# Kernel tuning notes

Measured on AMD Instinct MI355X. Metric: run time of the kernel, lower is better.

## Reference

```python
import jax, jax.numpy as jnp
import numpy as np
from jax import lax

OC = 128
KH, KW = 2, 2


def setup_inputs() -> dict:
    key = jax.random.key(0)
    k1, k2, k3 = jax.random.split(key, 3)
    C = 256
    n = C * KH * KW
    stdv = 1.0 / np.sqrt(n)
    x = jax.random.normal(k1, (16, C, 64, 64), dtype=jnp.float32)
    # original allocates (oc^2*kh*kw, C, kh, kw) but only uses first oc*kh*kw rows
    weight = jax.random.uniform(k2, (OC * OC * KH * KW, C, KH, KW), dtype=jnp.float32,
                                minval=-stdv, maxval=stdv)
    bias = jax.random.uniform(k3, (OC * (KH + KW),), dtype=jnp.float32,
                              minval=-stdv, maxval=stdv)
    return {"x": x, "weight": weight, "bias": bias}


def _robin_shuffle(x, weight, bias):
    # output[b,z,p,q] = stride-1 valid conv at (p,q) using filter
    # index (p%KH)*KW + (q%KW) + z*KH*KW, plus matching bias.
    nf = OC * KH * KW
    w = weight[:nf]  # (nf, C, KH, KW)
    full = lax.conv_general_dilated(
        x, w, window_strides=(1, 1), padding='VALID',
        dimension_numbers=('NCHW', 'OIHW', 'NCHW'))  # (N, nf, H', W')
    full = full + bias[:nf][None, :, None, None]
    N, _, Hp, Wp = full.shape
    full = full.reshape(N, OC, KH * KW, Hp, Wp)
    idx = (jnp.arange(Hp)[:, None] % KH) * KW + (jnp.arange(Wp)[None, :] % KW)  # (H', W')
    out = jnp.take_along_axis(full, idx[None, None, None, :, :], axis=2)
    return out.squeeze(2)  # (N, OC, H', W')


def reference(x, weight, bias):
    return _robin_shuffle(x, weight, bias)
```

## Files before the change

kernel.cpp:

```cpp
#include <hip/hip_runtime.h>

typedef __bf16 v8bf __attribute__((ext_vector_type(8)));
typedef float f32x4 __attribute__((ext_vector_type(4)));

#define C_IN 256
#define HW   64
#define OHW  63
#define NOC  128

__global__ void wprep(const float* __restrict__ w, __bf16* __restrict__ Wf) {
  int f = blockIdx.x;
  int c = threadIdx.x;
  f32x4 v = *(const f32x4*)(w + (size_t)f * 1024 + c * 4);
  int oc = f >> 2, kp = f & 3;
#pragma unroll
  for (int khkw = 0; khkw < 4; ++khkw)
    Wf[(((size_t)(kp * 4 + khkw) * 32 + (c >> 3)) * 128 + oc) * 8 + (c & 7)] =
        (__bf16)v[khkw];
}

__global__ __launch_bounds__(1024, 4) void robin_main(
    const float* __restrict__ x, const __bf16* __restrict__ Wf,
    const float* __restrict__ bias, float* __restrict__ out) {
  __shared__ __align__(16) __bf16 xs[2][5 * 33 * 64];
  char* xb0 = (char*)xs[0];
  char* xb1 = (char*)xs[1];

  const int tid  = threadIdx.x;
  const int lane = tid & 63;
  const int wid  = tid >> 6;
  const int hb   = blockIdx.x;
  const int n    = blockIdx.y;
  const int h0   = hb * 4;

  const int ocg  = wid >> 2;
  const int kp   = wid & 3;
  const int ph   = kp >> 1, pw = kp & 1;
  const int lcol = lane & 15;
  const int lg   = lane >> 4;

  if (tid < 80) {
    int g  = tid & 7;
    int t2 = tid >> 3;
    int dy = t2 % 5, bi = t2 / 5;
    f32x4 z = {0.f, 0.f, 0.f, 0.f};
    *(f32x4*)((bi ? xb1 : xb0) + (dy * 33 + 32) * 128 + g * 16) = z;
  }

  int boff[4];
#pragma unroll
  for (int khkw = 0; khkw < 4; ++khkw) {
    int kh = khkw >> 1, kw = khkw & 1;
    int dy0  = ph + kh;
    int wcol = 2 * lcol + pw + kw;
    int wp_  = wcol >> 1;
    boff[khkw] = ((dy0 * 33 + wp_) * 128 + (wcol & 1) * 64 + lg * 16) ^
                 ((wp_ & 7) << 4);
  }

  f32x4 acc[2][4];
#pragma unroll
  for (int m = 0; m < 2; ++m)
#pragma unroll
    for (int f = 0; f < 4; ++f) acc[m][f] = (f32x4){0.f, 0.f, 0.f, 0.f};

  const float* xbase = x + (size_t)n * C_IN * HW * HW;
  f32x4 xr[3];
  v8bf  a_reg[4][2];

#define A_LOAD(QQ)                                                             \
  {                                                                            \
    _Pragma("unroll") for (int khkw = 0; khkw < 4; ++khkw) {                   \
      const __bf16* wp =                                                       \
          Wf + (((size_t)(kp * 4 + khkw) * 32 + (QQ) * 4 + lg) * 128 +        \
                ocg * 32 + lcol) * 8;                                          \
      a_reg[khkw][0] = *(const v8bf*)wp;                                       \
      a_reg[khkw][1] = *(const v8bf*)(wp + 128);                               \
    }                                                                          \
  }

#define LOADQ(QQ)                                                              \
  {                                                                            \
    const int cbase = (QQ) * 32;                                               \
    _Pragma("unroll") for (int k = 0; k < 3; ++k) {                            \
      int v = k * 1024 + tid;                                                  \
      if (v < 2560) {                                                          \
        int w4 = v & 15, c = (v >> 4) & 31, dy = v >> 9;                       \
        int y = h0 + dy;                                                       \
        if (y < HW)                                                            \
          xr[k] = *(const f32x4*)(xbase + ((size_t)(cbase + c) * HW + y) * HW +\
                                  w4 * 4);                                     \
        else                                                                   \
          xr[k] = (f32x4){0.f, 0.f, 0.f, 0.f};                                 \
      }                                                                        \
    }                                                                          \
  }

#define WRITEQ(QQ)                                                             \
  {                                                                            \
    char* xd = ((QQ) & 1) ? xb1 : xb0;                                         \
    _Pragma("unroll") for (int k = 0; k < 3; ++k) {                            \
      int v = k * 1024 + tid;                                                  \
      if (v < 2560) {                                                          \
        int w4 = v & 15, c = (v >> 4) & 31, dy = v >> 9;                       \
        _Pragma("unroll") for (int j = 0; j < 4; ++j) {                        \
          int wcol = w4 * 4 + j;                                               \
          int wp_  = wcol >> 1;                                                \
          int bo = ((dy * 33 + wp_) * 128 + (wcol & 1) * 64 + c * 2) ^         \
                   ((wp_ & 7) << 4);                                           \
          *(__bf16*)(xd + bo) = (__bf16)xr[k][j];                              \
        }                                                                      \
      }                                                                        \
    }                                                                          \
  }

  LOADQ(0);
  WRITEQ(0);
  __syncthreads();

  for (int q = 0; q < 8; ++q) {
    A_LOAD(q);
    if (q < 7) LOADQ(q + 1);

    {
      const char* xsb = (q & 1) ? xb1 : xb0;
#pragma unroll
      for (int khkw = 0; khkw < 4; ++khkw) {
        v8bf b[4];
#pragma unroll
        for (int r = 0; r < 2; ++r)
#pragma unroll
          for (int hh = 0; hh < 2; ++hh)
            b[r * 2 + hh] =
                *(const v8bf*)(xsb + boff[khkw] + r * 8448 + hh * 2048);

#pragma unroll
        for (int m = 0; m < 2; ++m)
#pragma unroll
          for (int f = 0; f < 4; ++f)
            acc[m][f] = __builtin_amdgcn_mfma_f32_16x16x32_bf16(
                a_reg[khkw][m], b[f], acc[m][f], 0, 0, 0);
      }
    }

    if (q < 7) {
      WRITEQ(q + 1);
      __syncthreads();
    }
  }

#pragma unroll
  for (int m = 0; m < 2; ++m) {
#pragma unroll
    for (int r = 0; r < 2; ++r) {
      const int h = h0 + 2 * r + ph;
#pragma unroll
      for (int hh = 0; hh < 2; ++hh) {
        const int w = 2 * (hh * 16 + lcol) + pw;
        f32x4 v = acc[m][r * 2 + hh];
        if (h < OHW && w < OHW) {
#pragma unroll
          for (int reg = 0; reg < 4; ++reg) {
            int oc = ocg * 32 + m * 16 + lg * 4 + reg;
            out[((size_t)(n * NOC + oc) * OHW + h) * OHW + w] =
                v[reg] + bias[oc * 4 + kp];
          }
        }
      }
    }
  }
#undef A_LOAD
#undef LOADQ
#undef WRITEQ
}

extern "C" void kernel_launch(void* const* d_in, const int* in_sizes, int n_in,
                              void* d_out, int out_size, void* d_ws, size_t ws_size,
                              hipStream_t stream) {
  const float* x      = (const float*)d_in[0];
  const float* weight = (const float*)d_in[1];
  const float* bias   = (const float*)d_in[2];
  float* out          = (float*)d_out;
  __bf16* Wf          = (__bf16*)d_ws;

  wprep<<<512, 256, 0, stream>>>(weight, Wf);
  robin_main<<<dim3(16, 16), 1024, 0, stream>>>(x, Wf, bias, out);
}
```

Before: 44.65 us.

## Halve row strip per block, widen per-wave OC tile, raise MFMA priority

Each block now covers a 2-row strip (3 input rows staged in LDS) with 512 threads. Each wave computes 64 output channels instead of 32, so it holds 4 A fragments and needs only 2 B fragments per tap. The grid doubles to 32x16 blocks, which is meant to improve occupancy and load balance across CUs. The cost is more halo re-reading of input rows and more weight reloads per output. s_setprio is raised around the MFMA bursts.

```diff
diff --git a/kernel.cpp b/kernel.cpp
--- a/kernel.cpp
+++ b/kernel.cpp
@@ -19,19 +19,19 @@
         (__bf16)v[khkw];
 }
 
-__global__ __launch_bounds__(1024, 4) void robin_main(
+__global__ __launch_bounds__(512, 4) void robin_main(
     const float* __restrict__ x, const __bf16* __restrict__ Wf,
     const float* __restrict__ bias, float* __restrict__ out) {
-  __shared__ __align__(16) __bf16 xs[2][5 * 33 * 64];
+  __shared__ __align__(16) __bf16 xs[2][3 * 33 * 64];
   char* xb0 = (char*)xs[0];
   char* xb1 = (char*)xs[1];
 
-  const int tid  = threadIdx.x;
-  const int lane = tid & 63;
-  const int wid  = tid >> 6;
-  const int hb   = blockIdx.x;
-  const int n    = blockIdx.y;
-  const int h0   = hb * 4;
+  const int tid   = threadIdx.x;
+  const int lane  = tid & 63;
+  const int wid   = tid >> 6;
+  const int strip = blockIdx.x;
+  const int n     = blockIdx.y;
+  const int h0    = strip * 2;
 
   const int ocg  = wid >> 2;
   const int kp   = wid & 3;
@@ -39,43 +39,44 @@
   const int lcol = lane & 15;
   const int lg   = lane >> 4;
 
-  if (tid < 80) {
-    int g  = tid & 7;
-    int t2 = tid >> 3;
-    int dy = t2 % 5, bi = t2 / 5;
+  if (tid < 48) {
+    int bi = tid / 24, r2 = tid % 24;
+    int k = r2 >> 3, g = r2 & 7;
     f32x4 z = {0.f, 0.f, 0.f, 0.f};
-    *(f32x4*)((bi ? xb1 : xb0) + (dy * 33 + 32) * 128 + g * 16) = z;
+    *(f32x4*)((bi ? xb1 : xb0) + (k * 33 + 32) * 128 + g * 16) = z;
   }
 
   int boff[4];
 #pragma unroll
   for (int khkw = 0; khkw < 4; ++khkw) {
     int kh = khkw >> 1, kw = khkw & 1;
-    int dy0  = ph + kh;
+    int dy   = ph + kh;
     int wcol = 2 * lcol + pw + kw;
     int wp_  = wcol >> 1;
-    boff[khkw] = ((dy0 * 33 + wp_) * 128 + (wcol & 1) * 64 + lg * 16) ^
+    boff[khkw] = ((dy * 33 + wp_) * 128 + (wcol & 1) * 64 + lg * 16) ^
                  ((wp_ & 7) << 4);
   }
 
-  f32x4 acc[2][4];
+  f32x4 acc[4][2];
 #pragma unroll
-  for (int m = 0; m < 2; ++m)
+  for (int m = 0; m < 4; ++m)
 #pragma unroll
-    for (int f = 0; f < 4; ++f) acc[m][f] = (f32x4){0.f, 0.f, 0.f, 0.f};
+    for (int f = 0; f < 2; ++f) acc[m][f] = (f32x4){0.f, 0.f, 0.f, 0.f};
 
   const float* xbase = x + (size_t)n * C_IN * HW * HW;
+  const int s_c  = tid >> 4;
+  const int s_w4 = tid & 15;
   f32x4 xr[3];
-  v8bf  a_reg[4][2];
+  v8bf  a_reg[4][4];
 
 #define A_LOAD(QQ)                                                             \
   {                                                                            \
     _Pragma("unroll") for (int khkw = 0; khkw < 4; ++khkw) {                   \
       const __bf16* wp =                                                       \
           Wf + (((size_t)(kp * 4 + khkw) * 32 + (QQ) * 4 + lg) * 128 +        \
-                ocg * 32 + lcol) * 8;                                          \
-      a_reg[khkw][0] = *(const v8bf*)wp;                                       \
-      a_reg[khkw][1] = *(const v8bf*)(wp + 128);                               \
+                ocg * 64 + lcol) * 8;                                          \
+      _Pragma("unroll") for (int m = 0; m < 4; ++m)                            \
+          a_reg[khkw][m] = *(const v8bf*)(wp + m * 128);                       \
     }                                                                          \
   }
 
@@ -83,16 +84,12 @@
   {                                                                            \
     const int cbase = (QQ) * 32;                                               \
     _Pragma("unroll") for (int k = 0; k < 3; ++k) {                            \
-      int v = k * 1024 + tid;                                                  \
-      if (v < 2560) {                                                          \
-        int w4 = v & 15, c = (v >> 4) & 31, dy = v >> 9;                       \
-        int y = h0 + dy;                                                       \
-        if (y < HW)                                                            \
-          xr[k] = *(const f32x4*)(xbase + ((size_t)(cbase + c) * HW + y) * HW +\
-                                  w4 * 4);                                     \
-        else                                                                   \
-          xr[k] = (f32x4){0.f, 0.f, 0.f, 0.f};                                 \
-      }                                                                        \
+      int y = h0 + k;                                                          \
+      if (y < HW)                                                              \
+        xr[k] = *(const f32x4*)(xbase + ((size_t)(cbase + s_c) * HW + y) * HW +\
+                                s_w4 * 4);                                     \
+      else                                                                     \
+        xr[k] = (f32x4){0.f, 0.f, 0.f, 0.f};                                   \
     }                                                                          \
   }
 
@@ -100,16 +97,12 @@
   {                                                                            \
     char* xd = ((QQ) & 1) ? xb1 : xb0;                                         \
     _Pragma("unroll") for (int k = 0; k < 3; ++k) {                            \
-      int v = k * 1024 + tid;                                                  \
-      if (v < 2560) {                                                          \
-        int w4 = v & 15, c = (v >> 4) & 31, dy = v >> 9;                       \
-        _Pragma("unroll") for (int j = 0; j < 4; ++j) {                        \
-          int wcol = w4 * 4 + j;                                               \
-          int wp_  = wcol >> 1;                                                \
-          int bo = ((dy * 33 + wp_) * 128 + (wcol & 1) * 64 + c * 2) ^         \
-                   ((wp_ & 7) << 4);                                           \
-          *(__bf16*)(xd + bo) = (__bf16)xr[k][j];                              \
-        }                                                                      \
+      _Pragma("unroll") for (int j = 0; j < 4; ++j) {                          \
+        int wcol = s_w4 * 4 + j;                                               \
+        int wp_  = wcol >> 1;                                                  \
+        int bo = ((k * 33 + wp_) * 128 + (wcol & 1) * 64 + s_c * 2) ^          \
+                 ((wp_ & 7) << 4);                                             \
+        *(__bf16*)(xd + bo) = (__bf16)xr[k][j];                                \
       }                                                                        \
     }                                                                          \
   }
@@ -126,20 +119,19 @@
       const char* xsb = (q & 1) ? xb1 : xb0;
 #pragma unroll
       for (int khkw = 0; khkw < 4; ++khkw) {
-        v8bf b[4];
+        v8bf b[2];
 #pragma unroll
-        for (int r = 0; r < 2; ++r)
+        for (int hh = 0; hh < 2; ++hh)
+          b[hh] = *(const v8bf*)(xsb + boff[khkw] + hh * 2048);
+
+        __builtin_amdgcn_s_setprio(1);
 #pragma unroll
-          for (int hh = 0; hh < 2; ++hh)
-            b[r * 2 + hh] =
-                *(const v8bf*)(xsb + boff[khkw] + r * 8448 + hh * 2048);
-
+        for (int m = 0; m < 4; ++m)
 #pragma unroll
-        for (int m = 0; m < 2; ++m)
-#pragma unroll
-          for (int f = 0; f < 4; ++f)
+          for (int f = 0; f < 2; ++f)
             acc[m][f] = __builtin_amdgcn_mfma_f32_16x16x32_bf16(
                 a_reg[khkw][m], b[f], acc[m][f], 0, 0, 0);
+        __builtin_amdgcn_s_setprio(0);
       }
     }
 
@@ -149,19 +141,18 @@
     }
   }
 
+  const int h = h0 + ph;
+  if (h < OHW) {
 #pragma unroll
-  for (int m = 0; m < 2; ++m) {
-#pragma unroll
-    for (int r = 0; r < 2; ++r) {
-      const int h = h0 + 2 * r + ph;
+    for (int m = 0; m < 4; ++m) {
 #pragma unroll
       for (int hh = 0; hh < 2; ++hh) {
         const int w = 2 * (hh * 16 + lcol) + pw;
-        f32x4 v = acc[m][r * 2 + hh];
-        if (h < OHW && w < OHW) {
+        f32x4 v = acc[m][hh];
+        if (w < OHW) {
 #pragma unroll
           for (int reg = 0; reg < 4; ++reg) {
-            int oc = ocg * 32 + m * 16 + lg * 4 + reg;
+            int oc = ocg * 64 + m * 16 + lg * 4 + reg;
             out[((size_t)(n * NOC + oc) * OHW + h) * OHW + w] =
                 v[reg] + bias[oc * 4 + kp];
           }
@@ -184,5 +175,5 @@
   __bf16* Wf          = (__bf16*)d_ws;
 
   wprep<<<512, 256, 0, stream>>>(weight, Wf);
-  robin_main<<<dim3(16, 16), 1024, 0, stream>>>(x, Wf, bias, out);
+  robin_main<<<dim3(32, 16), 512, 0, stream>>>(x, Wf, bias, out);
 }
```

New measurement: 79.65 us. +78.4%, slower.

## Deepen global-to-register prefetch to two stages with fully unrolled channel loop

Applied to the files above, without the earlier changes.

Adds a second register staging buffer so global loads for chunk q+2 are issued while chunk q is computed and chunk q+1 is written to LDS. The channel loop is fully unrolled so the compiler can pick buffers statically. This hides more global-load latency at the cost of 12 extra VGPRs per thread, which may lower occupancy under the 1024x4 launch bounds or cause spills.

```diff
diff --git a/kernel.cpp b/kernel.cpp
--- a/kernel.cpp
+++ b/kernel.cpp
@@ -65,7 +65,7 @@
     for (int f = 0; f < 4; ++f) acc[m][f] = (f32x4){0.f, 0.f, 0.f, 0.f};
 
   const float* xbase = x + (size_t)n * C_IN * HW * HW;
-  f32x4 xr[3];
+  f32x4 xrA[3], xrB[3];
   v8bf  a_reg[4][2];
 
 #define A_LOAD(QQ)                                                             \
@@ -79,7 +79,7 @@
     }                                                                          \
   }
 
-#define LOADQ(QQ)                                                              \
+#define LOADQ(QQ, XR)                                                          \
   {                                                                            \
     const int cbase = (QQ) * 32;                                               \
     _Pragma("unroll") for (int k = 0; k < 3; ++k) {                            \
@@ -88,15 +88,15 @@
         int w4 = v & 15, c = (v >> 4) & 31, dy = v >> 9;                       \
         int y = h0 + dy;                                                       \
         if (y < HW)                                                            \
-          xr[k] = *(const f32x4*)(xbase + ((size_t)(cbase + c) * HW + y) * HW +\
+          XR[k] = *(const f32x4*)(xbase + ((size_t)(cbase + c) * HW + y) * HW +\
                                   w4 * 4);                                     \
         else                                                                   \
-          xr[k] = (f32x4){0.f, 0.f, 0.f, 0.f};                                 \
+          XR[k] = (f32x4){0.f, 0.f, 0.f, 0.f};                                 \
       }                                                                        \
     }                                                                          \
   }
 
-#define WRITEQ(QQ)                                                             \
+#define WRITEQ(QQ, XR)                                                         \
   {                                                                            \
     char* xd = ((QQ) & 1) ? xb1 : xb0;                                         \
     _Pragma("unroll") for (int k = 0; k < 3; ++k) {                            \
@@ -108,46 +108,52 @@
           int wp_  = wcol >> 1;                                                \
           int bo = ((dy * 33 + wp_) * 128 + (wcol & 1) * 64 + c * 2) ^         \
                    ((wp_ & 7) << 4);                                           \
-          *(__bf16*)(xd + bo) = (__bf16)xr[k][j];                              \
+          *(__bf16*)(xd + bo) = (__bf16)XR[k][j];                              \
         }                                                                      \
       }                                                                        \
     }                                                                          \
   }
 
-  LOADQ(0);
-  WRITEQ(0);
+#define COMPUTE(QQ)                                                            \
+  {                                                                            \
+    const char* xsb = ((QQ) & 1) ? xb1 : xb0;                                  \
+    _Pragma("unroll") for (int khkw = 0; khkw < 4; ++khkw) {                   \
+      v8bf b[4];                                                               \
+      _Pragma("unroll") for (int r = 0; r < 2; ++r)                            \
+        _Pragma("unroll") for (int hh = 0; hh < 2; ++hh)                       \
+          b[r * 2 + hh] =                                                      \
+              *(const v8bf*)(xsb + boff[khkw] + r * 8448 + hh * 2048);         \
+      _Pragma("unroll") for (int m = 0; m < 2; ++m)                            \
+        _Pragma("unroll") for (int f = 0; f < 4; ++f)                          \
+          acc[m][f] = __builtin_amdgcn_mfma_f32_16x16x32_bf16(                 \
+              a_reg[khkw][m], b[f], acc[m][f], 0, 0, 0);                       \
+    }                                                                          \
+  }
+
+#define ITER(QQ, XRL, XRW)                                                     \
+  {                                                                            \
+    A_LOAD(QQ);                    \
+    if ((QQ) < 6) LOADQ((QQ) + 2, XRL);        \
+    COMPUTE(QQ);                                                               \
+    if ((QQ) < 7) {                                                            \
+      WRITEQ((QQ) + 1, XRW);             \
+      __syncthreads();                                                         \
+    }                                                                          \
+  }
+
+  LOADQ(0, xrA);
+  LOADQ(1, xrB);
+  WRITEQ(0, xrA);
   __syncthreads();
 
-  for (int q = 0; q < 8; ++q) {
-    A_LOAD(q);
-    if (q < 7) LOADQ(q + 1);
-
-    {
-      const char* xsb = (q & 1) ? xb1 : xb0;
-#pragma unroll
-      for (int khkw = 0; khkw < 4; ++khkw) {
-        v8bf b[4];
-#pragma unroll
-        for (int r = 0; r < 2; ++r)
-#pragma unroll
-          for (int hh = 0; hh < 2; ++hh)
-            b[r * 2 + hh] =
-                *(const v8bf*)(xsb + boff[khkw] + r * 8448 + hh * 2048);
-
-#pragma unroll
-        for (int m = 0; m < 2; ++m)
-#pragma unroll
-          for (int f = 0; f < 4; ++f)
-            acc[m][f] = __builtin_amdgcn_mfma_f32_16x16x32_bf16(
-                a_reg[khkw][m], b[f], acc[m][f], 0, 0, 0);
-      }
-    }
-
-    if (q < 7) {
-      WRITEQ(q + 1);
-      __syncthreads();
-    }
-  }
+  ITER(0, xrA, xrB);
+  ITER(1, xrB, xrA);
+  ITER(2, xrA, xrB);
+  ITER(3, xrB, xrA);
+  ITER(4, xrA, xrB);
+  ITER(5, xrB, xrA);
+  ITER(6, xrA, xrB);
+  ITER(7, xrB, xrA);
 
 #pragma unroll
   for (int m = 0; m < 2; ++m) {
@@ -172,6 +178,8 @@
 #undef A_LOAD
 #undef LOADQ
 #undef WRITEQ
+#undef COMPUTE
+#undef ITER
 }
 
 extern "C" void kernel_launch(void* const* d_in, const int* in_sizes, int n_in,
```

Result: slower. 49.55 us (+11.0%).

## Pre-convert input to swizzled bf16 layout and stream tiles via direct global-to-LDS loads

Applied to the files above, without the earlier changes.

Adds an xprep kernel that converts x to bf16 once, packed and swizzled into the exact layout the main kernel's LDS tiles use. The main kernel then fills its double-buffered LDS with global_load_lds 16-byte transfers instead of loading fp32 into registers and scattering per-element bf16 stores. This removes register staging and many narrow LDS writes from the main loop. In exchange it adds an extra kernel launch plus a full write and re-read of the converted input through global memory, and edge columns are clamped rather than zero-padded.

```diff
diff --git a/kernel.cpp b/kernel.cpp
--- a/kernel.cpp
+++ b/kernel.cpp
@@ -2,6 +2,8 @@
 
 typedef __bf16 v8bf __attribute__((ext_vector_type(8)));
 typedef float f32x4 __attribute__((ext_vector_type(4)));
+typedef unsigned int u32;
+typedef unsigned int u32x4 __attribute__((ext_vector_type(4)));
 
 #define C_IN 256
 #define HW   64
@@ -19,12 +21,43 @@
         (__bf16)v[khkw];
 }
 
+__global__ __launch_bounds__(256) void xprep(const float* __restrict__ x,
+                                             __bf16* __restrict__ xp) {
+  int u = blockIdx.x * 4 + (threadIdx.x >> 6);
+  int lane = threadIdx.x & 63;
+  int y = u & 63, q = (u >> 6) & 7, n = u >> 9;
+  int w4 = lane & 15;
+  int co = lane >> 4;
+  const float* src =
+      x + (((size_t)(n * 256 + q * 32 + co * 8) * 64 + y) * 64) + w4 * 4;
+  f32x4 xv[8];
+#pragma unroll
+  for (int j = 0; j < 8; ++j) xv[j] = *(const f32x4*)(src + (size_t)j * 4096);
+  char* dst = (char*)xp + (((size_t)(n * 8 + q) * 64 + y) * 4096) + co * 16;
+#pragma unroll
+  for (int ww = 0; ww < 4; ++ww) {
+    int w_ = w4 * 4 + ww;
+    u32x4 pk;
+#pragma unroll
+    for (int k = 0; k < 4; ++k) {
+      u32 lo = (u32)__builtin_bit_cast(unsigned short, (__bf16)xv[2 * k][ww]);
+      u32 hi = (u32)__builtin_bit_cast(unsigned short, (__bf16)xv[2 * k + 1][ww]);
+      pk[k] = lo | (hi << 16);
+    }
+    *(u32x4*)(dst + (w_ >> 1) * 128 + (w_ & 1) * 64) = pk;
+  }
+}
+
+__device__ __forceinline__ void gl_lds16(const void* g, void* l) {
+  __builtin_amdgcn_global_load_lds(
+      (const __attribute__((address_space(1))) u32*)g,
+      (__attribute__((address_space(3))) u32*)l, 16, 0, 0);
+}
+
 __global__ __launch_bounds__(1024, 4) void robin_main(
-    const float* __restrict__ x, const __bf16* __restrict__ Wf,
+    const __bf16* __restrict__ xp, const __bf16* __restrict__ Wf,
     const float* __restrict__ bias, float* __restrict__ out) {
-  __shared__ __align__(16) __bf16 xs[2][5 * 33 * 64];
-  char* xb0 = (char*)xs[0];
-  char* xb1 = (char*)xs[1];
+  __shared__ __align__(16) char xs[2][20480];
 
   const int tid  = threadIdx.x;
   const int lane = tid & 63;
@@ -39,23 +72,21 @@
   const int lcol = lane & 15;
   const int lg   = lane >> 4;
 
-  if (tid < 80) {
-    int g  = tid & 7;
-    int t2 = tid >> 3;
-    int dy = t2 % 5, bi = t2 / 5;
-    f32x4 z = {0.f, 0.f, 0.f, 0.f};
-    *(f32x4*)((bi ? xb1 : xb0) + (dy * 33 + 32) * 128 + g * 16) = z;
-  }
+  const int lsub = ((lane >> 3) * 128) + (((lane & 7) * 16) ^ ((lane >> 3) << 4));
 
-  int boff[4];
+  int boff2[4][2];
 #pragma unroll
   for (int khkw = 0; khkw < 4; ++khkw) {
     int kh = khkw >> 1, kw = khkw & 1;
-    int dy0  = ph + kh;
-    int wcol = 2 * lcol + pw + kw;
-    int wp_  = wcol >> 1;
-    boff[khkw] = ((dy0 * 33 + wp_) * 128 + (wcol & 1) * 64 + lg * 16) ^
-                 ((wp_ & 7) << 4);
+    int dy0 = ph + kh;
+#pragma unroll
+    for (int hh = 0; hh < 2; ++hh) {
+      int wcol = 2 * (hh * 16 + lcol) + pw + kw;
+      if (wcol > 63) wcol = 63;
+      int wp = wcol >> 1;
+      boff2[khkw][hh] = dy0 * 4096 +
+          ((wp * 128 + (wcol & 1) * 64 + lg * 16) ^ ((wp & 7) << 4));
+    }
   }
 
   f32x4 acc[2][4];
@@ -64,89 +95,61 @@
 #pragma unroll
     for (int f = 0; f < 4; ++f) acc[m][f] = (f32x4){0.f, 0.f, 0.f, 0.f};
 
-  const float* xbase = x + (size_t)n * C_IN * HW * HW;
-  f32x4 xr[3];
-  v8bf  a_reg[4][2];
+  v8bf a_reg[4][2];
+  const char* xpc = (const char*)xp;
 
 #define A_LOAD(QQ)                                                             \
   {                                                                            \
     _Pragma("unroll") for (int khkw = 0; khkw < 4; ++khkw) {                   \
-      const __bf16* wp =                                                       \
+      const __bf16* wp_ =                                                      \
           Wf + (((size_t)(kp * 4 + khkw) * 32 + (QQ) * 4 + lg) * 128 +        \
                 ocg * 32 + lcol) * 8;                                          \
-      a_reg[khkw][0] = *(const v8bf*)wp;                                       \
-      a_reg[khkw][1] = *(const v8bf*)(wp + 128);                               \
+      a_reg[khkw][0] = *(const v8bf*)wp_;                                      \
+      a_reg[khkw][1] = *(const v8bf*)(wp_ + 128);                              \
     }                                                                          \
   }
 
-#define LOADQ(QQ)                                                              \
+#define ISSUE(QQ)                                                              \
   {                                                                            \
-    const int cbase = (QQ) * 32;                                               \
-    _Pragma("unroll") for (int k = 0; k < 3; ++k) {                            \
-      int v = k * 1024 + tid;                                                  \
-      if (v < 2560) {                                                          \
-        int w4 = v & 15, c = (v >> 4) & 31, dy = v >> 9;                       \
-        int y = h0 + dy;                                                       \
-        if (y < HW)                                                            \
-          xr[k] = *(const f32x4*)(xbase + ((size_t)(cbase + c) * HW + y) * HW +\
-                                  w4 * 4);                                     \
-        else                                                                   \
-          xr[k] = (f32x4){0.f, 0.f, 0.f, 0.f};                                 \
-      }                                                                        \
+    char* db = xs[(QQ) & 1];                                                   \
+    const char* sb = xpc + (((size_t)n * 8 + (QQ)) * 64) * 4096;               \
+    {                                                                          \
+      int dy = wid >> 2, wq = wid & 3;                                         \
+      int y = h0 + dy;                             \
+      gl_lds16(sb + (size_t)y * 4096 + wq * 1024 + lsub,                       \
+               db + dy * 4096 + wq * 1024);                                    \
+    }                                                                          \
+    if (wid < 4) {                                                             \
+      int y = h0 + 4; if (y > 63) y = 63;                                      \
+      gl_lds16(sb + (size_t)y * 4096 + wid * 1024 + lsub,                      \
+               db + 4 * 4096 + wid * 1024);                                    \
     }                                                                          \
   }
 
-#define WRITEQ(QQ)                                                             \
+#define COMPUTE(QQ)                                                            \
   {                                                                            \
-    char* xd = ((QQ) & 1) ? xb1 : xb0;                                         \
-    _Pragma("unroll") for (int k = 0; k < 3; ++k) {                            \
-      int v = k * 1024 + tid;                                                  \
-      if (v < 2560) {                                                          \
-        int w4 = v & 15, c = (v >> 4) & 31, dy = v >> 9;                       \
-        _Pragma("unroll") for (int j = 0; j < 4; ++j) {                        \
-          int wcol = w4 * 4 + j;                                               \
-          int wp_  = wcol >> 1;                                                \
-          int bo = ((dy * 33 + wp_) * 128 + (wcol & 1) * 64 + c * 2) ^         \
-                   ((wp_ & 7) << 4);                                           \
-          *(__bf16*)(xd + bo) = (__bf16)xr[k][j];                              \
-        }                                                                      \
-      }                                                                        \
+    const char* xsb = xs[(QQ) & 1];                                            \
+    _Pragma("unroll") for (int khkw = 0; khkw < 4; ++khkw) {                   \
+      v8bf b[4];                                                               \
+      _Pragma("unroll") for (int r = 0; r < 2; ++r)                            \
+        _Pragma("unroll") for (int hh = 0; hh < 2; ++hh)                       \
+          b[r * 2 + hh] =                                                      \
+              *(const v8bf*)(xsb + boff2[khkw][hh] + r * 8192);                \
+      _Pragma("unroll") for (int m = 0; m < 2; ++m)                            \
+        _Pragma("unroll") for (int f = 0; f < 4; ++f)                          \
+          acc[m][f] = __builtin_amdgcn_mfma_f32_16x16x32_bf16(                 \
+              a_reg[khkw][m], b[f], acc[m][f], 0, 0, 0);                       \
     }                                                                          \
   }
 
-  LOADQ(0);
-  WRITEQ(0);
+  ISSUE(0);
   __syncthreads();
 
   for (int q = 0; q < 8; ++q) {
     A_LOAD(q);
-    if (q < 7) LOADQ(q + 1);
-
-    {
-      const char* xsb = (q & 1) ? xb1 : xb0;
-#pragma unroll
-      for (int khkw = 0; khkw < 4; ++khkw) {
-        v8bf b[4];
-#pragma unroll
-        for (int r = 0; r < 2; ++r)
-#pragma unroll
-          for (int hh = 0; hh < 2; ++hh)
-            b[r * 2 + hh] =
-                *(const v8bf*)(xsb + boff[khkw] + r * 8448 + hh * 2048);
-
-#pragma unroll
-        for (int m = 0; m < 2; ++m)
-#pragma unroll
-          for (int f = 0; f < 4; ++f)
-            acc[m][f] = __builtin_amdgcn_mfma_f32_16x16x32_bf16(
-                a_reg[khkw][m], b[f], acc[m][f], 0, 0, 0);
-      }
-    }
-
-    if (q < 7) {
-      WRITEQ(q + 1);
-      __syncthreads();
-    }
+    if (q < 7) ISSUE(q + 1);
+    COMPUTE(q);
+    if (q < 7) __syncthreads();
   }
 
 #pragma unroll
@@ -170,8 +173,8 @@
     }
   }
 #undef A_LOAD
-#undef LOADQ
-#undef WRITEQ
+#undef ISSUE
+#undef COMPUTE
 }
 
 extern "C" void kernel_launch(void* const* d_in, const int* in_sizes, int n_in,
@@ -181,8 +184,10 @@
   const float* weight = (const float*)d_in[1];
   const float* bias   = (const float*)d_in[2];
   float* out          = (float*)d_out;
-  __bf16* Wf          = (__bf16*)d_ws;
+  __bf16* Wf = (__bf16*)d_ws;
+  __bf16* xp = (__bf16*)((char*)d_ws + (1 << 20));
 
   wprep<<<512, 256, 0, stream>>>(weight, Wf);
-  robin_main<<<dim3(16, 16), 1024, 0, stream>>>(x, Wf, bias, out);
+  xprep<<<2048, 256, 0, stream>>>(x, xp);
+  robin_main<<<dim3(16, 16), 1024, 0, stream>>>(xp, Wf, bias, out);
 }
```

New measurement: 54.63 us (median of 2 runs). 22.4% more time.
